# Kernel optimization log

Measured on AMD Instinct MI355X. Metric: run time of the kernel, lower is better.

## Reference

```python
import jax, jax.numpy as jnp
import numpy as np

EPS = 1e-5
B, M, N, D = 8, 4096, 1024, 1024


def setup_inputs() -> dict:
    key = jax.random.key(0)
    kx, kw, kb, kg, kbe = jax.random.split(key, 5)
    return {
        "x": jax.random.normal(kx, (B, M, N), dtype=jnp.float32),
        "w": jax.random.normal(kw, (N, D), dtype=jnp.float32) * 0.02,
        "b": jax.random.normal(kb, (D,), dtype=jnp.float32) * 0.02,
        "gamma": jax.random.uniform(kg, (N,), dtype=jnp.float32, minval=0.5, maxval=1.5),
        "beta": jax.random.normal(kbe, (N,), dtype=jnp.float32) * 0.02,
    }


def reference(x, w, b, gamma, beta):
    # Fused LayerNorm (over last dim, biased variance, eps=1e-5) + matmul + bias.
    mean = jnp.mean(x, axis=-1, keepdims=True)                 # [B,M,1]
    var = jnp.mean(jnp.square(x - mean), axis=-1, keepdims=True)
    rstd = jax.lax.rsqrt(var + EPS)                            # [B,M,1]
    ln = (x - mean) * rstd * gamma + beta                      # [B,M,N]
    return jnp.einsum('bmn,nd->bmd', ln, w) + b                # [B,M,D]
```

## Files before the change

kernel.cpp:

```cpp
#include <hip/hip_runtime.h>
#include <stdint.h>

#define RROWS 32768
#define KDIM  1024
#define DDIM  1024

typedef __bf16 bf16;
typedef __bf16 bf16x4 __attribute__((ext_vector_type(4)));
typedef __bf16 bf16x8 __attribute__((ext_vector_type(8)));
typedef float  f32x4  __attribute__((ext_vector_type(4)));

typedef __attribute__((address_space(1))) const unsigned int* gas_ptr;
typedef __attribute__((address_space(3))) unsigned int* las_ptr;

__global__ __launch_bounds__(256) void prep_gt(const float* __restrict__ w,
                                               const float* __restrict__ gamma,
                                               bf16* __restrict__ Gt) {
    __shared__ float tile[64][65];
    const int k0 = blockIdx.x * 64;
    const int d0 = blockIdx.y * 64;
    const int t  = threadIdx.x;
    const int col4 = (t & 15) * 4;
    const int rowb = t >> 4;
#pragma unroll
    for (int r = 0; r < 4; ++r) {
        const int k = rowb + r * 16;
        const float4 v = *(const float4*)&w[(size_t)(k0 + k) * DDIM + d0 + col4];
        const float g = gamma[k0 + k];
        tile[k][col4 + 0] = v.x * g;
        tile[k][col4 + 1] = v.y * g;
        tile[k][col4 + 2] = v.z * g;
        tile[k][col4 + 3] = v.w * g;
    }
    __syncthreads();
#pragma unroll
    for (int r = 0; r < 2; ++r) {
        const int d  = (t >> 3) + r * 32;
        const int ks = (t & 7) * 8;
        bf16x8 o;
#pragma unroll
        for (int j = 0; j < 8; ++j) o[j] = (bf16)tile[ks + j][d];
        *(bf16x8*)&Gt[(size_t)(d0 + d) * KDIM + k0 + ks] = o;
    }
}

__global__ __launch_bounds__(256) void prep_part(const float* __restrict__ w,
                                                 const float* __restrict__ gamma,
                                                 const float* __restrict__ beta,
                                                 float* __restrict__ partG,
                                                 float* __restrict__ partB) {
    const int d  = blockIdx.x * 256 + threadIdx.x;
    const int kc = blockIdx.y;
    float ag = 0.f, ab = 0.f;
    for (int k = kc * 64; k < kc * 64 + 64; ++k) {
        const float wv = w[(size_t)k * DDIM + d];
        ag += gamma[k] * wv;
        ab += beta[k] * wv;
    }
    partG[(size_t)kc * DDIM + d] = ag;
    partB[(size_t)kc * DDIM + d] = ab;
}

__global__ __launch_bounds__(256) void prep_reduce(const float* __restrict__ partG,
                                                   const float* __restrict__ partB,
                                                   const float* __restrict__ b,
                                                   float* __restrict__ gw,
                                                   float* __restrict__ cvec) {
    const int d = blockIdx.x * 256 + threadIdx.x;
    float g = 0.f, a = 0.f;
#pragma unroll
    for (int j = 0; j < 16; ++j) {
        g += partG[(size_t)j * DDIM + d];
        a += partB[(size_t)j * DDIM + d];
    }
    gw[d]   = g;
    cvec[d] = a + b[d];
}

__global__ __launch_bounds__(256) void ln_convert(const float* __restrict__ x,
                                                  bf16* __restrict__ xb) {
    const int wave = threadIdx.x >> 6;
    const int lane = threadIdx.x & 63;
    const int row  = blockIdx.x * 4 + wave;
    const float4* xr = (const float4*)(x + (size_t)row * KDIM);

    float4 v[4];
    float s1 = 0.f, s2 = 0.f;
#pragma unroll
    for (int j = 0; j < 4; ++j) {
        v[j] = xr[lane + j * 64];
        s1 += v[j].x + v[j].y + v[j].z + v[j].w;
        s2 += v[j].x * v[j].x + v[j].y * v[j].y + v[j].z * v[j].z + v[j].w * v[j].w;
    }
#pragma unroll
    for (int ofs = 1; ofs < 64; ofs <<= 1) {
        s1 += __shfl_xor(s1, ofs, 64);
        s2 += __shfl_xor(s2, ofs, 64);
    }
    const float mean = s1 * (1.0f / KDIM);
    const float var  = s2 * (1.0f / KDIM) - mean * mean;
    const float rstd = rsqrtf(var + 1e-5f);

    bf16x4* xo = (bf16x4*)(xb + (size_t)row * KDIM);
#pragma unroll
    for (int j = 0; j < 4; ++j) {
        bf16x4 o;
        o[0] = (bf16)((v[j].x - mean) * rstd);
        o[1] = (bf16)((v[j].y - mean) * rstd);
        o[2] = (bf16)((v[j].z - mean) * rstd);
        o[3] = (bf16)((v[j].w - mean) * rstd);
        xo[lane + j * 64] = o;
    }
}

#define BM 128
#define BN 128
#define BK 64

__global__ __launch_bounds__(256) void gemm_bt(const bf16* __restrict__ xb,
                                               const bf16* __restrict__ Gt,
                                               const float* __restrict__ cvec,
                                               float* __restrict__ out) {
    __shared__ __align__(16) bf16 As[BM * BK];
    __shared__ __align__(16) bf16 Bs[BN * BK];

    const int t     = threadIdx.x;
    const int dTile = blockIdx.x;
    const int mTile = blockIdx.y;
    const int row0  = mTile * BM;
    const int col0  = dTile * BN;

    const int wave = t >> 6;
    const int lane = t & 63;
    const int wr   = wave >> 1;
    const int wc   = wave & 1;
    const int quad = lane >> 4;
    const int r16  = lane & 15;

    f32x4 acc[4][4];
#pragma unroll
    for (int i = 0; i < 4; ++i)
#pragma unroll
        for (int j = 0; j < 4; ++j) acc[i][j] = (f32x4)0.0f;

    for (int k0 = 0; k0 < KDIM; k0 += BK) {
        __syncthreads();

#pragma unroll
        for (int j = 0; j < 4; ++j) {
            const int ci   = j * 256 + t;
            const int row  = ci >> 3;
            const int slot = ci & 7;
            const int q    = slot ^ (row & 7);
            const bf16* gp = xb + (size_t)(row0 + row) * KDIM + k0 + q * 8;
            char* lp = (char*)As + ci * 16;
            __builtin_amdgcn_global_load_lds((gas_ptr)(const void*)gp,
                                             (las_ptr)(void*)lp, 16, 0, 0);
        }
#pragma unroll
        for (int j = 0; j < 4; ++j) {
            const int ci   = j * 256 + t;
            const int row  = ci >> 3;
            const int slot = ci & 7;
            const int q    = slot ^ (row & 7);
            const bf16* gp = Gt + (size_t)(col0 + row) * KDIM + k0 + q * 8;
            char* lp = (char*)Bs + ci * 16;
            __builtin_amdgcn_global_load_lds((gas_ptr)(const void*)gp,
                                             (las_ptr)(void*)lp, 16, 0, 0);
        }

        __syncthreads();

#pragma unroll
        for (int kk = 0; kk < 2; ++kk) {
            bf16x8 af[4], bfr[4];
#pragma unroll
            for (int i = 0; i < 4; ++i) {
                const int row  = wr * 64 + i * 16 + r16;
                const int slot = (kk * 4 + quad) ^ (row & 7);
                af[i] = *(const bf16x8*)&As[row * BK + slot * 8];
            }
#pragma unroll
            for (int j = 0; j < 4; ++j) {
                const int row  = wc * 64 + j * 16 + r16;
                const int slot = (kk * 4 + quad) ^ (row & 7);
                bfr[j] = *(const bf16x8*)&Bs[row * BK + slot * 8];
            }
#pragma unroll
            for (int i = 0; i < 4; ++i)
#pragma unroll
                for (int j = 0; j < 4; ++j)
                    acc[i][j] = __builtin_amdgcn_mfma_f32_16x16x32_bf16(af[i], bfr[j], acc[i][j], 0, 0, 0);
        }
    }

    const int lr = quad * 4;
    const int lc = r16;
#pragma unroll
    for (int j = 0; j < 4; ++j) {
        const int col = col0 + wc * 64 + j * 16 + lc;
        const float cv = cvec[col];
#pragma unroll
        for (int i = 0; i < 4; ++i) {
#pragma unroll
            for (int rg = 0; rg < 4; ++rg) {
                const int row = row0 + wr * 64 + i * 16 + lr + rg;
                out[(size_t)row * DDIM + col] = acc[i][j][rg] + cv;
            }
        }
    }
}

#define FBK 32
#define APAD 40

__global__ __launch_bounds__(256) void fused_gemm(const float* __restrict__ x,
                                                  const bf16* __restrict__ Gt,
                                                  const float* __restrict__ gw,
                                                  const float* __restrict__ cvec,
                                                  float* __restrict__ out) {
    __shared__ __align__(16) bf16 As2[BM * APAD];
    __shared__ __align__(16) bf16 Bs2[BM * FBK];
    __shared__ float meanS[BM];
    __shared__ float rstdS[BM];

    const int t     = threadIdx.x;
    const int mTile = blockIdx.x;
    const int dTile = blockIdx.y;
    const int row0  = mTile * BM;
    const int col0  = dTile * BN;
    const int wave = t >> 6;
    const int lane = t & 63;
    const int wr   = wave >> 1;
    const int wc   = wave & 1;
    const int a_row = t >> 3;
    const int a_seg = t & 7;

    float s1[4] = {0.f, 0.f, 0.f, 0.f};
    float s2[4] = {0.f, 0.f, 0.f, 0.f};
    f32x4 acc[4][4];
#pragma unroll
    for (int i = 0; i < 4; ++i)
#pragma unroll
        for (int j = 0; j < 4; ++j) acc[i][j] = (f32x4)0.0f;

    for (int k0 = 0; k0 < KDIM; k0 += FBK) {
        __syncthreads();
#pragma unroll
        for (int j = 0; j < 2; ++j) {
            const int off  = j * 4096 + t * 16;
            const int brow = off >> 6;
            const int kseg = (off & 63) >> 1;
            const bf16* gp = Gt + (size_t)(col0 + brow) * KDIM + k0 + kseg;
            char* lp = (char*)Bs2 + off;
            __builtin_amdgcn_global_load_lds((gas_ptr)(const void*)gp,
                                             (las_ptr)(void*)lp, 16, 0, 0);
        }
#pragma unroll
        for (int r = 0; r < 4; ++r) {
            const int row = r * 32 + a_row;
            const float4 v = *(const float4*)&x[(size_t)(row0 + row) * KDIM + k0 + a_seg * 4];
            s1[r] += v.x + v.y + v.z + v.w;
            s2[r] += v.x * v.x + v.y * v.y + v.z * v.z + v.w * v.w;
            bf16x4 pk;
            pk[0] = (bf16)v.x; pk[1] = (bf16)v.y; pk[2] = (bf16)v.z; pk[3] = (bf16)v.w;
            *(bf16x4*)&As2[row * APAD + a_seg * 4] = pk;
        }
        __syncthreads();

        bf16x8 af[4], bfr[4];
        const int arow = wr * 64 + (lane & 15);
        const int brow = wc * 64 + (lane & 15);
        const int koff = (lane >> 4) * 8;
#pragma unroll
        for (int i = 0; i < 4; ++i)
            af[i] = *(const bf16x8*)&As2[(arow + i * 16) * APAD + koff];
#pragma unroll
        for (int j = 0; j < 4; ++j)
            bfr[j] = *(const bf16x8*)&Bs2[(brow + j * 16) * FBK + koff];
#pragma unroll
        for (int i = 0; i < 4; ++i)
#pragma unroll
            for (int j = 0; j < 4; ++j)
                acc[i][j] = __builtin_amdgcn_mfma_f32_16x16x32_bf16(af[i], bfr[j], acc[i][j], 0, 0, 0);
    }

#pragma unroll
    for (int r = 0; r < 4; ++r) {
        float a = s1[r], b = s2[r];
#pragma unroll
        for (int ofs = 1; ofs < 8; ofs <<= 1) {
            a += __shfl_xor(a, ofs, 64);
            b += __shfl_xor(b, ofs, 64);
        }
        if (a_seg == 0) {
            const int row = r * 32 + a_row;
            const float mean = a * (1.0f / KDIM);
            const float var  = b * (1.0f / KDIM) - mean * mean;
            meanS[row] = mean;
            rstdS[row] = rsqrtf(var + 1e-5f);
        }
    }
    __syncthreads();

    const int lr = (lane >> 4) * 4;
    const int lc = lane & 15;
#pragma unroll
    for (int j = 0; j < 4; ++j) {
        const int col = col0 + wc * 64 + j * 16 + lc;
        const float gwv = gw[col];
        const float cv  = cvec[col];
#pragma unroll
        for (int i = 0; i < 4; ++i) {
#pragma unroll
            for (int rg = 0; rg < 4; ++rg) {
                const int rowL = wr * 64 + i * 16 + lr + rg;
                const float vv = rstdS[rowL] * (acc[i][j][rg] - meanS[rowL] * gwv) + cv;
                out[(size_t)(row0 + rowL) * DDIM + col] = vv;
            }
        }
    }
}

extern "C" void kernel_launch(void* const* d_in, const int* in_sizes, int n_in,
                              void* d_out, int out_size, void* d_ws, size_t ws_size,
                              hipStream_t stream) {
    const float* x     = (const float*)d_in[0];
    const float* w     = (const float*)d_in[1];
    const float* b     = (const float*)d_in[2];
    const float* gamma = (const float*)d_in[3];
    const float* beta  = (const float*)d_in[4];
    float* out = (float*)d_out;

    char* ws = (char*)d_ws;
    const size_t XB_B = (size_t)RROWS * KDIM * sizeof(bf16);
    bf16*  xb    = (bf16*)ws;
    bf16*  Gt    = (bf16*)(ws + XB_B);
    float* partG = (float*)(ws + XB_B + (2u << 20));
    float* partB = (float*)(ws + XB_B + (2u << 20) + (64u << 10));
    float* gw    = (float*)(ws + XB_B + (2u << 20) + (128u << 10));
    float* cvec  = (float*)(ws + XB_B + (2u << 20) + (132u << 10));

    const bool big_ws = ws_size >= XB_B + (3u << 20);

    if (big_ws) {
        prep_gt<<<dim3(16, 16), 256, 0, stream>>>(w, gamma, Gt);
        prep_part<<<dim3(4, 16), 256, 0, stream>>>(w, gamma, beta, partG, partB);
        prep_reduce<<<4, 256, 0, stream>>>(partG, partB, b, gw, cvec);
        ln_convert<<<RROWS / 4, 256, 0, stream>>>(x, xb);
        gemm_bt<<<dim3(8, 256), 256, 0, stream>>>(xb, Gt, cvec, out);
    } else {
        bf16*  Gt2    = (bf16*)ws;
        float* partG2 = (float*)(ws + (2u << 20));
        float* partB2 = (float*)(ws + (2u << 20) + (64u << 10));
        float* gw2    = (float*)(ws + (2u << 20) + (128u << 10));
        float* cvec2  = (float*)(ws + (2u << 20) + (132u << 10));
        prep_gt<<<dim3(16, 16), 256, 0, stream>>>(w, gamma, Gt2);
        prep_part<<<dim3(4, 16), 256, 0, stream>>>(w, gamma, beta, partG2, partB2);
        prep_reduce<<<4, 256, 0, stream>>>(partG2, partB2, b, gw2, cvec2);
        fused_gemm<<<dim3(256, 8), 256, 0, stream>>>(x, Gt2, gw2, cvec2, out);
    }
}
```

Before: 337.7 us.

## Replace 128x128 GEMM with double-buffered 256x256 tile kernel using 8 waves

Replaces the single-buffered 128x128x64 bf16 GEMM with a 256x256-tile, 512-thread kernel. It double-buffers the A and B tiles in LDS using direct global-to-LDS loads issued in half-K chunks, so the next k-step's loads overlap the current MFMAs. It also raises MFMA priority with s_setprio and remaps block IDs so neighbouring blocks share tiles in cache. Larger tiles halve the global traffic per FLOP, but the kernel now needs 128 accumulator registers per thread, many barriers and hand-written vmcnt waits whose correctness depends on exact load ordering.

```diff
diff --git a/kernel.cpp b/kernel.cpp
--- a/kernel.cpp
+++ b/kernel.cpp
@@ -113,104 +113,143 @@
     }
 }
 
+__device__ __forceinline__ void stage_half(const bf16* __restrict__ g0,
+                                           bf16* lregion, int kt, int h, int tid) {
+#pragma unroll
+    for (int j = 0; j < 2; ++j) {
+        const int ci = j * 512 + tid;
+        const int r  = ci >> 2;
+        const int qs = (ci & 3) ^ (r & 3);
+        const bf16* gp = g0 + (size_t)r * KDIM + kt * 64 + h * 32 + qs * 8;
+        char* lp = (char*)lregion + ci * 16;
+        __builtin_amdgcn_global_load_lds((gas_ptr)(const void*)gp,
+                                         (las_ptr)(void*)lp, 16, 0, 0);
+    }
+}
+
+__device__ __forceinline__ bf16x8 ld_frag(const bf16* region, int r, int g) {
+    return *(const bf16x8*)(region + r * 32 + ((g ^ (r & 3)) * 8));
+}
+
+#define MFMA_QUAD(MOFF)                                                         \
+    __builtin_amdgcn_s_setprio(1);                                              \
+    _Pragma("unroll")                                                           \
+    for (int m_ = 0; m_ < 4; ++m_) {                                            \
+        _Pragma("unroll")                                                       \
+        for (int n_ = 0; n_ < 4; ++n_)                                          \
+            acc[(MOFF) + m_][n_] = __builtin_amdgcn_mfma_f32_16x16x32_bf16(     \
+                af[m_], bfr[n_], acc[(MOFF) + m_][n_], 0, 0, 0);                \
+    }                                                                           \
+    __builtin_amdgcn_s_setprio(0);
+
+__global__ __launch_bounds__(512, 2) void gemm256(const bf16* __restrict__ xb,
+                                                  const bf16* __restrict__ Gt,
+                                                  const float* __restrict__ cvec,
+                                                  float* __restrict__ out) {
+    __shared__ __align__(16) bf16 As[2][2][8192];
+    __shared__ __align__(16) bf16 Bs[2][2][8192];
+
+    const int tid  = threadIdx.x;
+    const int bid  = blockIdx.x;
+    const int wg   = (bid & 7) * 64 + (bid >> 3);
+    const int mT   = wg >> 2;
+    const int dT   = wg & 3;
+    const int row0 = mT * 256;
+    const int col0 = dT * 256;
+
+    const int wave = tid >> 6;
+    const int lane = tid & 63;
+    const int wm   = wave >> 2;
+    const int wn   = wave & 3;
+    const int r16  = lane & 15;
+    const int g    = lane >> 4;
+
+    const bf16* aG = xb + (size_t)row0 * KDIM;
+    const bf16* bG = Gt + (size_t)col0 * KDIM;
+
+    f32x4 acc[8][4];
+#pragma unroll
+    for (int m = 0; m < 8; ++m)
+#pragma unroll
+        for (int n = 0; n < 4; ++n) acc[m][n] = (f32x4)0.0f;
+
+    stage_half(aG, &As[0][0][0], 0, 0, tid);
+    stage_half(bG, &Bs[0][0][0], 0, 0, tid);
+    stage_half(aG, &As[0][1][0], 0, 1, tid);
+    stage_half(bG, &Bs[0][1][0], 0, 1, tid);
+    asm volatile("s_waitcnt vmcnt(4)" ::: "memory");
+    __builtin_amdgcn_s_barrier();
+
+    bf16x8 af[4], bfr[4];
+    for (int t = 0; t < 16; ++t) {
+        const int  c  = t & 1;
+        const int  o  = c ^ 1;
+        const bool st = (t < 15);
+        const bf16* A0 = &As[c][0][0];
+        const bf16* A1 = &As[c][1][0];
+        const bf16* B0 = &Bs[c][0][0];
+        const bf16* B1 = &Bs[c][1][0];
+        const int am = wm * 128 + r16;
+        const int bn = wn * 64 + r16;
+
+#pragma unroll
+        for (int m = 0; m < 4; ++m) af[m] = ld_frag(A0, am + m * 16, g);
+#pragma unroll
+        for (int n = 0; n < 4; ++n) bfr[n] = ld_frag(B0, bn + n * 16, g);
+        if (st) stage_half(aG, &As[o][0][0], t + 1, 0, tid);
+        __builtin_amdgcn_s_barrier();
+        MFMA_QUAD(0)
+        __builtin_amdgcn_s_barrier();
+
+#pragma unroll
+        for (int m = 0; m < 4; ++m) af[m] = ld_frag(A0, am + 64 + m * 16, g);
+        if (st) {
+            stage_half(bG, &Bs[o][0][0], t + 1, 0, tid);
+            asm volatile("s_waitcnt vmcnt(4)" ::: "memory");
+        } else {
+            asm volatile("s_waitcnt vmcnt(0)" ::: "memory");
+        }
+        __builtin_amdgcn_s_barrier();
+        MFMA_QUAD(4)
+        __builtin_amdgcn_s_barrier();
+
+#pragma unroll
+        for (int m = 0; m < 4; ++m) af[m] = ld_frag(A1, am + m * 16, g);
+#pragma unroll
+        for (int n = 0; n < 4; ++n) bfr[n] = ld_frag(B1, bn + n * 16, g);
+        if (st) stage_half(aG, &As[o][1][0], t + 1, 1, tid);
+        __builtin_amdgcn_s_barrier();
+        MFMA_QUAD(0)
+        __builtin_amdgcn_s_barrier();
+
+#pragma unroll
+        for (int m = 0; m < 4; ++m) af[m] = ld_frag(A1, am + 64 + m * 16, g);
+        if (st) {
+            stage_half(bG, &Bs[o][1][0], t + 1, 1, tid);
+            asm volatile("s_waitcnt vmcnt(4)" ::: "memory");
+        }
+        __builtin_amdgcn_s_barrier();
+        MFMA_QUAD(4)
+        __builtin_amdgcn_s_barrier();
+    }
+
+#pragma unroll
+    for (int n = 0; n < 4; ++n) {
+        const int colL = wn * 64 + n * 16 + r16;
+        const float cv = cvec[col0 + colL];
+#pragma unroll
+        for (int m = 0; m < 8; ++m) {
+#pragma unroll
+            for (int rg = 0; rg < 4; ++rg) {
+                const int rowL = wm * 128 + m * 16 + g * 4 + rg;
+                out[(size_t)(row0 + rowL) * DDIM + col0 + colL] = acc[m][n][rg] + cv;
+            }
+        }
+    }
+}
+
 #define BM 128
 #define BN 128
-#define BK 64
-
-__global__ __launch_bounds__(256) void gemm_bt(const bf16* __restrict__ xb,
-                                               const bf16* __restrict__ Gt,
-                                               const float* __restrict__ cvec,
-                                               float* __restrict__ out) {
-    __shared__ __align__(16) bf16 As[BM * BK];
-    __shared__ __align__(16) bf16 Bs[BN * BK];
-
-    const int t     = threadIdx.x;
-    const int dTile = blockIdx.x;
-    const int mTile = blockIdx.y;
-    const int row0  = mTile * BM;
-    const int col0  = dTile * BN;
-
-    const int wave = t >> 6;
-    const int lane = t & 63;
-    const int wr   = wave >> 1;
-    const int wc   = wave & 1;
-    const int quad = lane >> 4;
-    const int r16  = lane & 15;
-
-    f32x4 acc[4][4];
-#pragma unroll
-    for (int i = 0; i < 4; ++i)
-#pragma unroll
-        for (int j = 0; j < 4; ++j) acc[i][j] = (f32x4)0.0f;
-
-    for (int k0 = 0; k0 < KDIM; k0 += BK) {
-        __syncthreads();
-
-#pragma unroll
-        for (int j = 0; j < 4; ++j) {
-            const int ci   = j * 256 + t;
-            const int row  = ci >> 3;
-            const int slot = ci & 7;
-            const int q    = slot ^ (row & 7);
-            const bf16* gp = xb + (size_t)(row0 + row) * KDIM + k0 + q * 8;
-            char* lp = (char*)As + ci * 16;
-            __builtin_amdgcn_global_load_lds((gas_ptr)(const void*)gp,
-                                             (las_ptr)(void*)lp, 16, 0, 0);
-        }
-#pragma unroll
-        for (int j = 0; j < 4; ++j) {
-            const int ci   = j * 256 + t;
-            const int row  = ci >> 3;
-            const int slot = ci & 7;
-            const int q    = slot ^ (row & 7);
-            const bf16* gp = Gt + (size_t)(col0 + row) * KDIM + k0 + q * 8;
-            char* lp = (char*)Bs + ci * 16;
-            __builtin_amdgcn_global_load_lds((gas_ptr)(const void*)gp,
-                                             (las_ptr)(void*)lp, 16, 0, 0);
-        }
-
-        __syncthreads();
-
-#pragma unroll
-        for (int kk = 0; kk < 2; ++kk) {
-            bf16x8 af[4], bfr[4];
-#pragma unroll
-            for (int i = 0; i < 4; ++i) {
-                const int row  = wr * 64 + i * 16 + r16;
-                const int slot = (kk * 4 + quad) ^ (row & 7);
-                af[i] = *(const bf16x8*)&As[row * BK + slot * 8];
-            }
-#pragma unroll
-            for (int j = 0; j < 4; ++j) {
-                const int row  = wc * 64 + j * 16 + r16;
-                const int slot = (kk * 4 + quad) ^ (row & 7);
-                bfr[j] = *(const bf16x8*)&Bs[row * BK + slot * 8];
-            }
-#pragma unroll
-            for (int i = 0; i < 4; ++i)
-#pragma unroll
-                for (int j = 0; j < 4; ++j)
-                    acc[i][j] = __builtin_amdgcn_mfma_f32_16x16x32_bf16(af[i], bfr[j], acc[i][j], 0, 0, 0);
-        }
-    }
-
-    const int lr = quad * 4;
-    const int lc = r16;
-#pragma unroll
-    for (int j = 0; j < 4; ++j) {
-        const int col = col0 + wc * 64 + j * 16 + lc;
-        const float cv = cvec[col];
-#pragma unroll
-        for (int i = 0; i < 4; ++i) {
-#pragma unroll
-            for (int rg = 0; rg < 4; ++rg) {
-                const int row = row0 + wr * 64 + i * 16 + lr + rg;
-                out[(size_t)row * DDIM + col] = acc[i][j][rg] + cv;
-            }
-        }
-    }
-}
-
 #define FBK 32
 #define APAD 40
 
@@ -348,7 +387,7 @@
         prep_part<<<dim3(4, 16), 256, 0, stream>>>(w, gamma, beta, partG, partB);
         prep_reduce<<<4, 256, 0, stream>>>(partG, partB, b, gw, cvec);
         ln_convert<<<RROWS / 4, 256, 0, stream>>>(x, xb);
-        gemm_bt<<<dim3(8, 256), 256, 0, stream>>>(xb, Gt, cvec, out);
+        gemm256<<<dim3(512), 512, 0, stream>>>(xb, Gt, cvec, out);
     } else {
         bf16*  Gt2    = (bf16*)ws;
         float* partG2 = (float*)(ws + (2u << 20));
```

Result: no change. 337.2 us (-0.1%).
